# Kernel optimization log

Hardware: AMD Instinct MI355X
Metric: run time of the kernel (lower is better)

## Reference

```python
import jax, jax.numpy as jnp
import numpy as np
import math

N_NODES = 50000
N_EDGES = 800000
IN_DIM = 128
OUT_DIM = 64
TIME_DIM = 128


def setup_inputs() -> dict:
    key = jax.random.key(0)
    ks = jax.random.split(key, 9)
    return {
        "node_feats": jax.random.normal(ks[0], (N_NODES, IN_DIM), dtype=jnp.float32),
        "time_diff": jax.random.uniform(ks[1], (N_EDGES,), dtype=jnp.float32),
        "src": jax.random.randint(ks[2], (N_EDGES,), 0, N_NODES, dtype=jnp.int32),
        "dst": jax.random.randint(ks[3], (N_EDGES,), 0, N_NODES, dtype=jnp.int32),
        "W": jax.random.normal(ks[4], (OUT_DIM, IN_DIM), dtype=jnp.float32) * 0.05,
        "Wv": jax.random.normal(ks[5], (OUT_DIM, IN_DIM), dtype=jnp.float32) * 0.05,
        "omega": jax.random.normal(ks[6], (TIME_DIM // 2,), dtype=jnp.float32),
        "Wt": jax.random.normal(ks[7], (OUT_DIM, TIME_DIM), dtype=jnp.float32) * 0.05,
        "a": jax.random.normal(ks[8], (3 * OUT_DIM,), dtype=jnp.float32) * 0.05,
    }


def reference(node_feats, time_diff, src, dst, W, Wv, omega, Wt, a):
    N = node_feats.shape[0]
    d = W.shape[0]  # out_dim
    time_dim = 2 * omega.shape[0]

    # gather + linear projections per edge
    h_src = node_feats[src] @ W.T          # [E, d]
    h_dst = node_feats[dst] @ W.T          # [E, d]
    v_src = node_feats[src] @ Wv.T         # [E, d]

    # temporal encoding: interleaved sin/cos of t * omega, scaled by sqrt(1/dim)
    ang = time_diff[:, None] * omega[None, :]                       # [E, dim/2]
    pe = jnp.stack([jnp.sin(ang), jnp.cos(ang)], axis=-1)
    pe = pe.reshape(ang.shape[0], time_dim) * jnp.float32(math.sqrt(1.0 / time_dim))
    t_emb = pe @ Wt.T                                               # [E, d]

    # attn_fc(concat([h_src, h_dst, t_emb])) == split dot products (same math, no big concat)
    e = h_src @ a[:d] + h_dst @ a[d:2 * d] + t_emb @ a[2 * d:]      # [E]
    e = jnp.where(e > 0, e, 0.2 * e)  # LeakyReLU(0.2)

    # edge_softmax: softmax over incoming edges of each destination node
    m = jax.ops.segment_max(e, dst, num_segments=N)
    ex = jnp.exp(e - m[dst])
    den = jax.ops.segment_sum(ex, dst, num_segments=N)
    alpha = ex / den[dst]  # dropout is identity in eval mode

    # weighted message scatter-sum aggregation
    msg = v_src * alpha[:, None]                                    # [E, d]
    return jax.ops.segment_sum(msg, dst, num_segments=N)            # [N, d]
```

## Files before the change

### kernel.cpp

```cpp
#include <hip/hip_runtime.h>
#include <hip/hip_bf16.h>
#include <hip/hip_fp16.h>
#include <math.h>

#define IN_DIM   128
#define OUT_DIM  64
#define THALF    64
#define PE_SCALE 0.08838834764831845f
#define TBL      2048
#define EPB_LOG  14
#define EPB      (1 << EPB_LOG)

typedef __attribute__((ext_vector_type(8))) short  short8;
typedef __attribute__((ext_vector_type(4))) float  f32x4;

__device__ inline unsigned short bf16_rne(float x) {
    unsigned u = __float_as_uint(x);
    return (unsigned short)((u + 0x7FFFu + ((u >> 16) & 1u)) >> 16);
}

__global__ __launch_bounds__(256) void k_prep(
    const float* __restrict__ W, const float* __restrict__ Wt,
    const float* __restrict__ a, const float* __restrict__ Wv,
    const float* __restrict__ omega,
    float* __restrict__ gtab, unsigned short* __restrict__ Bp,
    int* __restrict__ pref)
{
    __shared__ float satv[IN_DIM];
    __shared__ float saW1[IN_DIM], saW2[IN_DIM];
    int t = threadIdx.x;
    if (t < IN_DIM) {
        float x3 = 0.f;
        for (int j = 0; j < OUT_DIM; ++j)
            x3 += a[2 * OUT_DIM + j] * Wt[j * IN_DIM + t];
        satv[t] = x3;
        if (blockIdx.x == 0) {
            float x1 = 0.f, x2 = 0.f;
            for (int j = 0; j < OUT_DIM; ++j) {
                float wj = W[j * IN_DIM + t];
                x1 += a[j] * wj;
                x2 += a[OUT_DIM + j] * wj;
            }
            saW1[t] = x1; saW2[t] = x2;
        }
    }
    __syncthreads();

    int idx = blockIdx.x * 256 + t;
    if (idx <= TBL) {
        float tt = (float)idx * (1.0f / TBL);
        float acc = 0.f;
#pragma unroll
        for (int i = 0; i < THALF; ++i) {
            float sp, cp;
            __sincosf(tt * omega[i], &sp, &cp);
            acc += sp * satv[2 * i] + cp * satv[2 * i + 1];
        }
        gtab[idx] = acc;
    }
    if (idx < 64) pref[idx] = 0;

    if (blockIdx.x == 0) {
        for (int i = t; i < 5 * 4 * 64 * 8; i += 256) {
            int j    = i & 7;
            int lane = (i >> 3) & 63;
            int k0i  = (i >> 9) & 3;
            int tt   = i >> 11;
            int kk = k0i * 32 + (lane >> 4) * 8 + j;
            int n  = lane & 15;
            float val;
            if (tt < 4)     val = Wv[(tt * 16 + n) * IN_DIM + kk];
            else            val = (n == 0) ? saW1[kk] : (n == 1) ? saW2[kk] : 0.f;
            Bp[i] = bf16_rne(val);
        }
    }
}

__global__ __launch_bounds__(1024) void k_hist(
    const int* __restrict__ dst,
    unsigned short* __restrict__ lrank,
    unsigned short* __restrict__ ghist16,
    int N, int E)
{
    extern __shared__ unsigned h[];
    int NH = (N + 1) >> 1;
    int t = threadIdx.x;
    for (int i = t; i < NH; i += 1024) h[i] = 0u;
    __syncthreads();
    int b = blockIdx.x;
    int e0 = b << EPB_LOG;
    int e1 = e0 + EPB; if (e1 > E) e1 = E;
    for (int e = e0 + t; e < e1; e += 1024) {
        int d = dst[e];
        unsigned inc = (d & 1) ? 0x10000u : 1u;
        unsigned old = atomicAdd(&h[d >> 1], inc);
        lrank[e] = (unsigned short)((d & 1) ? (old >> 16) : (old & 0xFFFFu));
    }
    __syncthreads();
    unsigned* gh32 = (unsigned*)(ghist16 + (size_t)b * N);
    for (int w = t; w < NH; w += 1024) gh32[w] = h[w];
}

__global__ __launch_bounds__(256) void k_scan_fuse(
    unsigned short* __restrict__ ghist16,
    int* __restrict__ offs,
    int* __restrict__ pref,
    int B, int N)
{
    __shared__ int lds[256];
    int b = blockIdx.x, t = threadIdx.x;
    int n0 = b * 1024 + t * 4;
    unsigned r0 = 0, r1 = 0, r2 = 0, r3 = 0;
    if (n0 + 3 < N) {
        for (int bb = 0; bb < B; ++bb) {
            unsigned short* p = ghist16 + (size_t)bb * N + n0;
            uint2 c = *(uint2*)p;
            uint2 w;
            w.x = (r0 & 0xFFFFu) | (r1 << 16);
            w.y = (r2 & 0xFFFFu) | (r3 << 16);
            *(uint2*)p = w;
            r0 += c.x & 0xFFFFu; r1 += c.x >> 16;
            r2 += c.y & 0xFFFFu; r3 += c.y >> 16;
        }
    } else if (n0 < N) {
        for (int bb = 0; bb < B; ++bb) {
            unsigned short* p = ghist16 + (size_t)bb * N + n0;
            unsigned c0 = p[0]; p[0] = (unsigned short)r0; r0 += c0;
            if (n0 + 1 < N) { unsigned c = p[1]; p[1] = (unsigned short)r1; r1 += c; }
            if (n0 + 2 < N) { unsigned c = p[2]; p[2] = (unsigned short)r2; r2 += c; }
            if (n0 + 3 < N) { unsigned c = p[3]; p[3] = (unsigned short)r3; r3 += c; }
        }
    }
    int s = (int)(r0 + r1 + r2 + r3);
    lds[t] = s;
    __syncthreads();
    for (int off = 1; off < 256; off <<= 1) {
        int tmp = (t >= off) ? lds[t - off] : 0;
        __syncthreads();
        lds[t] += tmp;
        __syncthreads();
    }
    int ex = lds[t] - s;
    if (n0 + 3 < N) {
        int4 o;
        o.x = ex;
        o.y = ex + (int)r0;
        o.z = ex + (int)(r0 + r1);
        o.w = ex + (int)(r0 + r1 + r2);
        *(int4*)(offs + n0) = o;
    } else if (n0 < N) {
        offs[n0] = ex;
        if (n0 + 1 < N) offs[n0 + 1] = ex + (int)r0;
        if (n0 + 2 < N) offs[n0 + 2] = ex + (int)(r0 + r1);
        if (n0 + 3 < N) offs[n0 + 3] = ex + (int)(r0 + r1 + r2);
    }
    int total = lds[255];
    if (t > b && t < (int)gridDim.x) atomicAdd(pref + t, total);
}

__global__ __launch_bounds__(256) void k_node_mfma(
    const float* __restrict__ feats,
    const unsigned short* __restrict__ Bp,
    unsigned short* __restrict__ vb,
    float* __restrict__ s1,
    float* __restrict__ s2,
    int N)
{
    int gwave = (blockIdx.x * 256 + threadIdx.x) >> 6;
    int lane  = threadIdx.x & 63;
    int ntiles = (N + 15) >> 4;
    if (gwave >= ntiles) return;
    int row = lane & 15, quad = lane >> 4;
    int nodeA = gwave * 16 + row;
    int nodeL = nodeA < N ? nodeA : N - 1;

    const float* arow = feats + (size_t)nodeL * IN_DIM + quad * 8;
    short8 afrag[4];
#pragma unroll
    for (int k0i = 0; k0i < 4; ++k0i) {
        float4 fa = *(const float4*)(arow + k0i * 32);
        float4 fb = *(const float4*)(arow + k0i * 32 + 4);
        union { unsigned u[4]; short8 s; } cv;
        cv.u[0] = (__float_as_uint(fa.x) >> 16) | (__float_as_uint(fa.y) & 0xFFFF0000u);
        cv.u[1] = (__float_as_uint(fa.z) >> 16) | (__float_as_uint(fa.w) & 0xFFFF0000u);
        cv.u[2] = (__float_as_uint(fb.x) >> 16) | (__float_as_uint(fb.y) & 0xFFFF0000u);
        cv.u[3] = (__float_as_uint(fb.z) >> 16) | (__float_as_uint(fb.w) & 0xFFFF0000u);
        afrag[k0i] = cv.s;
    }

    const short8* B8 = (const short8*)Bp;
    f32x4 acc[5];
#pragma unroll
    for (int t = 0; t < 5; ++t) acc[t] = (f32x4){0.f, 0.f, 0.f, 0.f};
#pragma unroll
    for (int t = 0; t < 5; ++t) {
#pragma unroll
        for (int k0i = 0; k0i < 4; ++k0i)
            acc[t] = __builtin_amdgcn_mfma_f32_16x16x32_bf16(
                afrag[k0i], B8[(t * 4 + k0i) * 64 + lane], acc[t], 0, 0, 0);
    }

    int col = lane & 15;
    int baseNode = gwave * 16 + quad * 4;
#pragma unroll
    for (int r = 0; r < 4; ++r) {
        int nd = baseNode + r;
        if (nd < N) {
            unsigned short* vr = vb + (size_t)nd * OUT_DIM + col;
#pragma unroll
            for (int t = 0; t < 4; ++t) vr[t * 16] = bf16_rne(acc[t][r]);
            if (col == 0)      s1[nd] = acc[4][r];
            else if (col == 1) s2[nd] = acc[4][r];
        }
    }
}

__global__ __launch_bounds__(256) void k_scatter_fused(
    const float* __restrict__ tdiff,
    const int* __restrict__ src,
    const int* __restrict__ dst,
    const float* __restrict__ gtab,
    const float* __restrict__ s1,
    const float* __restrict__ s2,
    const unsigned short* __restrict__ lrank,
    const unsigned short* __restrict__ ghist16,
    const int* __restrict__ offs,
    const int* __restrict__ pref,
    unsigned* __restrict__ payload,
    int N, int E)
{
    int base = (blockIdx.x * 256 + threadIdx.x) * 8;
    if (base >= E) return;
    if (base + 8 <= E) {
        int4   sa = *(const int4*)(src + base);
        int4   sb = *(const int4*)(src + base + 4);
        int4   da = *(const int4*)(dst + base);
        int4   db = *(const int4*)(dst + base + 4);
        float4 ta = *(const float4*)(tdiff + base);
        float4 tb = *(const float4*)(tdiff + base + 4);
        ushort4 la = *(const ushort4*)(lrank + base);
        ushort4 lb = *(const ushort4*)(lrank + base + 4);
        int s[8]    = {sa.x, sa.y, sa.z, sa.w, sb.x, sb.y, sb.z, sb.w};
        int d[8]    = {da.x, da.y, da.z, da.w, db.x, db.y, db.z, db.w};
        float tv[8] = {ta.x, ta.y, ta.z, ta.w, tb.x, tb.y, tb.z, tb.w};
        int lr[8]   = {la.x, la.y, la.z, la.w, lb.x, lb.y, lb.z, lb.w};

        int pos[8];
#pragma unroll
        for (int i = 0; i < 8; ++i) {
            int b = (base + i) >> EPB_LOG;
            pos[i] = offs[d[i]] + pref[d[i] >> 10] +
                     (int)ghist16[(size_t)b * N + d[i]] + lr[i];
        }
#pragma unroll
        for (int i = 0; i < 8; ++i) {
            float a1 = s1[s[i]];
            float a2 = s2[d[i]];
            float x = tv[i] * (float)TBL;
            int i0 = (int)x;
            i0 = i0 < 0 ? 0 : (i0 > TBL - 1 ? TBL - 1 : i0);
            float fr = x - (float)i0;
            float ev = a1 + a2 + PE_SCALE * (gtab[i0] + fr * (gtab[i0 + 1] - gtab[i0]));
            ev = ev > 0.f ? ev : 0.2f * ev;
            unsigned pw = ((unsigned)s[i] << 16) | (unsigned)__half_as_ushort(__float2half(ev));
            payload[pos[i]] = pw;
        }
    } else {
        for (int e = base; e < E; ++e) {
            int s = src[e], d = dst[e];
            float a1 = s1[s], a2 = s2[d];
            float x = tdiff[e] * (float)TBL;
            int i0 = (int)x;
            i0 = i0 < 0 ? 0 : (i0 > TBL - 1 ? TBL - 1 : i0);
            float fr = x - (float)i0;
            float ev = a1 + a2 + PE_SCALE * (gtab[i0] + fr * (gtab[i0 + 1] - gtab[i0]));
            ev = ev > 0.f ? ev : 0.2f * ev;
            unsigned pw = ((unsigned)s << 16) | (unsigned)__half_as_ushort(__float2half(ev));
            int b = e >> EPB_LOG;
            int pos = offs[d] + pref[d >> 10] + (int)ghist16[(size_t)b * N + d] + (int)lrank[e];
            payload[pos] = pw;
        }
    }
}

__global__ __launch_bounds__(256) void k_aggregate(
    const int* __restrict__ offs,
    const int* __restrict__ pref,
    const unsigned* __restrict__ payload,
    const unsigned short* __restrict__ vb,
    float* __restrict__ out,
    int N, int E)
{
    int wid  = (blockIdx.x * blockDim.x + threadIdx.x) >> 6;
    int lane = threadIdx.x & 63;
    if (wid >= N) return;
    int beg = offs[wid] + pref[wid >> 10];
    int end = (wid + 1 < N) ? (offs[wid + 1] + pref[(wid + 1) >> 10]) : E;
    int deg = end - beg;
    int g8 = lane >> 3, r = lane & 7;

    float acc[8];
#pragma unroll
    for (int i = 0; i < 8; ++i) acc[i] = 0.f;
    float den = 0.f;

    for (int base = 0; base < deg; base += 64) {
        int cl = deg - base; if (cl > 64) cl = 64;
        bool valid = lane < cl;
        unsigned pl = valid ? payload[beg + base + lane] : 0u;
        float ex = valid ? __expf(__half2float(__ushort_as_half((unsigned short)(pl & 0xFFFFu)))) : 0.f;
        int   sv = valid ? (int)(pl >> 16) : 0;

        float sum = ex;
#pragma unroll
        for (int off = 32; off; off >>= 1) sum += __shfl_xor(sum, off, 64);
        den += sum;

        int rounds = (cl + 15) >> 4;
        for (int j = 0; j < rounds; ++j) {
            int i0 = j * 16 + g8;
            int i1 = i0 + 8;
            float e0 = __shfl(ex, i0, 64);
            int   s0 = __shfl(sv, i0, 64);
            float e1 = __shfl(ex, i1, 64);
            int   s1v = __shfl(sv, i1, 64);
            uint4 w0 = *((const uint4*)(vb + (size_t)s0 * OUT_DIM) + r);
            uint4 w1 = *((const uint4*)(vb + (size_t)s1v * OUT_DIM) + r);
            acc[0] += e0 * __uint_as_float(w0.x << 16)         + e1 * __uint_as_float(w1.x << 16);
            acc[1] += e0 * __uint_as_float(w0.x & 0xFFFF0000u) + e1 * __uint_as_float(w1.x & 0xFFFF0000u);
            acc[2] += e0 * __uint_as_float(w0.y << 16)         + e1 * __uint_as_float(w1.y << 16);
            acc[3] += e0 * __uint_as_float(w0.y & 0xFFFF0000u) + e1 * __uint_as_float(w1.y & 0xFFFF0000u);
            acc[4] += e0 * __uint_as_float(w0.z << 16)         + e1 * __uint_as_float(w1.z << 16);
            acc[5] += e0 * __uint_as_float(w0.z & 0xFFFF0000u) + e1 * __uint_as_float(w1.z & 0xFFFF0000u);
            acc[6] += e0 * __uint_as_float(w0.w << 16)         + e1 * __uint_as_float(w1.w << 16);
            acc[7] += e0 * __uint_as_float(w0.w & 0xFFFF0000u) + e1 * __uint_as_float(w1.w & 0xFFFF0000u);
        }
    }

#pragma unroll
    for (int i = 0; i < 8; ++i) {
        acc[i] += __shfl_xor(acc[i], 8, 64);
        acc[i] += __shfl_xor(acc[i], 16, 64);
        acc[i] += __shfl_xor(acc[i], 32, 64);
    }

    if (g8 == 0) {
        float inv = (deg > 0) ? 1.f / den : 0.f;
        float* o = out + (size_t)wid * OUT_DIM + r * 8;
        *(float4*)(o)     = make_float4(acc[0] * inv, acc[1] * inv, acc[2] * inv, acc[3] * inv);
        *(float4*)(o + 4) = make_float4(acc[4] * inv, acc[5] * inv, acc[6] * inv, acc[7] * inv);
    }
}

extern "C" void kernel_launch(void* const* d_in, const int* in_sizes, int n_in,
                              void* d_out, int out_size, void* d_ws, size_t ws_size,
                              hipStream_t stream) {
    const float* feats = (const float*)d_in[0];
    const float* tdiff = (const float*)d_in[1];
    const int*   src   = (const int*)d_in[2];
    const int*   dst   = (const int*)d_in[3];
    const float* W     = (const float*)d_in[4];
    const float* Wv    = (const float*)d_in[5];
    const float* omega = (const float*)d_in[6];
    const float* Wt    = (const float*)d_in[7];
    const float* a     = (const float*)d_in[8];
    float* out = (float*)d_out;

    int N = in_sizes[0] / IN_DIM;
    int E = in_sizes[1];
    int B = (E + EPB - 1) >> EPB_LOG;

    float* ws      = (float*)d_ws;
    unsigned short* vb = (unsigned short*)ws;
    float* s1      = ws + (size_t)N * 32;
    float* s2      = s1 + N;
    unsigned* payload = (unsigned*)(s2 + N);
    unsigned short* lrank = (unsigned short*)(payload + E);
    int*   offs    = (int*)(lrank + ((E + 1) & ~1));
    int    offs_elems = ((N + 1023) / 1024) * 1024;
    int*   pref    = offs + offs_elems;
    float* gtab    = (float*)(pref + 64);
    unsigned short* Bp = (unsigned short*)(gtab + TBL + 1);
    size_t gho = ((size_t)((char*)(Bp + 10240) - (char*)ws) + 7) & ~(size_t)7;
    unsigned short* ghist16 = (unsigned short*)((char*)ws + gho);

    int nb = (N + 1023) / 1024;
    int ntiles = (N + 15) / 16;
    int eb8 = (E + 8 * 256 - 1) / (8 * 256);
    unsigned ldsb = (unsigned)(((N + 1) / 2) * 4);

    k_prep<<<(TBL / 256) + 1, 256, 0, stream>>>(W, Wt, a, Wv, omega, gtab, Bp, pref);
    k_hist<<<B, 1024, ldsb, stream>>>(dst, lrank, ghist16, N, E);
    k_node_mfma<<<(ntiles * 64 + 255) / 256, 256, 0, stream>>>(feats, Bp, vb, s1, s2, N);
    k_scan_fuse<<<nb, 256, 0, stream>>>(ghist16, offs, pref, B, N);
    k_scatter_fused<<<eb8, 256, 0, stream>>>(tdiff, src, dst, gtab, s1, s2,
                                             lrank, ghist16, offs, pref, payload, N, E);
    long long tot = (long long)N * OUT_DIM;
    k_aggregate<<<(int)((tot + 255) / 256), 256, 0, stream>>>(offs, pref, payload, vb, out, N, E);
}
```

Baseline: 181.7 us.

## Merge histogram and node MFMA kernels into one launch; fold denominator into gather loop

The destination histogram kernel and the per-node MFMA projection kernel are combined into one launch, with extra blocks beyond B running the projection. This removes one launch and lets the two independent phases overlap. The MFMA blocks now request the same large dynamic LDS allocation as the histogram blocks, which can limit occupancy. Separately, the aggregate kernel drops the per-chunk wave reduction of the softmax denominator, accumulates it per lane group inside the gather loop, and reduces it once at the end.

```diff
diff --git a/kernel.cpp b/kernel.cpp
--- a/kernel.cpp
+++ b/kernel.cpp
@@ -76,29 +76,84 @@
     }
 }
 
-__global__ __launch_bounds__(1024) void k_hist(
+__global__ __launch_bounds__(1024) void k_hist_mfma(
     const int* __restrict__ dst,
     unsigned short* __restrict__ lrank,
     unsigned short* __restrict__ ghist16,
-    int N, int E)
+    const float* __restrict__ feats,
+    const unsigned short* __restrict__ Bp,
+    unsigned short* __restrict__ vb,
+    float* __restrict__ s1,
+    float* __restrict__ s2,
+    int N, int E, int B)
 {
     extern __shared__ unsigned h[];
-    int NH = (N + 1) >> 1;
     int t = threadIdx.x;
-    for (int i = t; i < NH; i += 1024) h[i] = 0u;
-    __syncthreads();
-    int b = blockIdx.x;
-    int e0 = b << EPB_LOG;
-    int e1 = e0 + EPB; if (e1 > E) e1 = E;
-    for (int e = e0 + t; e < e1; e += 1024) {
-        int d = dst[e];
-        unsigned inc = (d & 1) ? 0x10000u : 1u;
-        unsigned old = atomicAdd(&h[d >> 1], inc);
-        lrank[e] = (unsigned short)((d & 1) ? (old >> 16) : (old & 0xFFFFu));
-    }
-    __syncthreads();
-    unsigned* gh32 = (unsigned*)(ghist16 + (size_t)b * N);
-    for (int w = t; w < NH; w += 1024) gh32[w] = h[w];
+    if ((int)blockIdx.x < B) {
+        int NH = (N + 1) >> 1;
+        for (int i = t; i < NH; i += 1024) h[i] = 0u;
+        __syncthreads();
+        int b = blockIdx.x;
+        int e0 = b << EPB_LOG;
+        int e1 = e0 + EPB; if (e1 > E) e1 = E;
+        for (int e = e0 + t; e < e1; e += 1024) {
+            int d = dst[e];
+            unsigned inc = (d & 1) ? 0x10000u : 1u;
+            unsigned old = atomicAdd(&h[d >> 1], inc);
+            lrank[e] = (unsigned short)((d & 1) ? (old >> 16) : (old & 0xFFFFu));
+        }
+        __syncthreads();
+        unsigned* gh32 = (unsigned*)(ghist16 + (size_t)b * N);
+        for (int w = t; w < NH; w += 1024) gh32[w] = h[w];
+        return;
+    }
+    int gwave = ((int)blockIdx.x - B) * 16 + (t >> 6);
+    int lane  = t & 63;
+    int ntiles = (N + 15) >> 4;
+    if (gwave >= ntiles) return;
+    int row = lane & 15, quad = lane >> 4;
+    int nodeA = gwave * 16 + row;
+    int nodeL = nodeA < N ? nodeA : N - 1;
+
+    const float* arow = feats + (size_t)nodeL * IN_DIM + quad * 8;
+    short8 afrag[4];
+#pragma unroll
+    for (int k0i = 0; k0i < 4; ++k0i) {
+        float4 fa = *(const float4*)(arow + k0i * 32);
+        float4 fb = *(const float4*)(arow + k0i * 32 + 4);
+        union { unsigned u[4]; short8 s; } cv;
+        cv.u[0] = (__float_as_uint(fa.x) >> 16) | (__float_as_uint(fa.y) & 0xFFFF0000u);
+        cv.u[1] = (__float_as_uint(fa.z) >> 16) | (__float_as_uint(fa.w) & 0xFFFF0000u);
+        cv.u[2] = (__float_as_uint(fb.x) >> 16) | (__float_as_uint(fb.y) & 0xFFFF0000u);
+        cv.u[3] = (__float_as_uint(fb.z) >> 16) | (__float_as_uint(fb.w) & 0xFFFF0000u);
+        afrag[k0i] = cv.s;
+    }
+
+    const short8* B8 = (const short8*)Bp;
+    f32x4 acc[5];
+#pragma unroll
+    for (int tt = 0; tt < 5; ++tt) acc[tt] = (f32x4){0.f, 0.f, 0.f, 0.f};
+#pragma unroll
+    for (int tt = 0; tt < 5; ++tt) {
+#pragma unroll
+        for (int k0i = 0; k0i < 4; ++k0i)
+            acc[tt] = __builtin_amdgcn_mfma_f32_16x16x32_bf16(
+                afrag[k0i], B8[(tt * 4 + k0i) * 64 + lane], acc[tt], 0, 0, 0);
+    }
+
+    int col = lane & 15;
+    int baseNode = gwave * 16 + quad * 4;
+#pragma unroll
+    for (int r = 0; r < 4; ++r) {
+        int nd = baseNode + r;
+        if (nd < N) {
+            unsigned short* vr = vb + (size_t)nd * OUT_DIM + col;
+#pragma unroll
+            for (int tt = 0; tt < 4; ++tt) vr[tt * 16] = bf16_rne(acc[tt][r]);
+            if (col == 0)      s1[nd] = acc[4][r];
+            else if (col == 1) s2[nd] = acc[4][r];
+        }
+    }
 }
 
 __global__ __launch_bounds__(256) void k_scan_fuse(
@@ -156,63 +211,6 @@
     }
     int total = lds[255];
     if (t > b && t < (int)gridDim.x) atomicAdd(pref + t, total);
-}
-
-__global__ __launch_bounds__(256) void k_node_mfma(
-    const float* __restrict__ feats,
-    const unsigned short* __restrict__ Bp,
-    unsigned short* __restrict__ vb,
-    float* __restrict__ s1,
-    float* __restrict__ s2,
-    int N)
-{
-    int gwave = (blockIdx.x * 256 + threadIdx.x) >> 6;
-    int lane  = threadIdx.x & 63;
-    int ntiles = (N + 15) >> 4;
-    if (gwave >= ntiles) return;
-    int row = lane & 15, quad = lane >> 4;
-    int nodeA = gwave * 16 + row;
-    int nodeL = nodeA < N ? nodeA : N - 1;
-
-    const float* arow = feats + (size_t)nodeL * IN_DIM + quad * 8;
-    short8 afrag[4];
-#pragma unroll
-    for (int k0i = 0; k0i < 4; ++k0i) {
-        float4 fa = *(const float4*)(arow + k0i * 32);
-        float4 fb = *(const float4*)(arow + k0i * 32 + 4);
-        union { unsigned u[4]; short8 s; } cv;
-        cv.u[0] = (__float_as_uint(fa.x) >> 16) | (__float_as_uint(fa.y) & 0xFFFF0000u);
-        cv.u[1] = (__float_as_uint(fa.z) >> 16) | (__float_as_uint(fa.w) & 0xFFFF0000u);
-        cv.u[2] = (__float_as_uint(fb.x) >> 16) | (__float_as_uint(fb.y) & 0xFFFF0000u);
-        cv.u[3] = (__float_as_uint(fb.z) >> 16) | (__float_as_uint(fb.w) & 0xFFFF0000u);
-        afrag[k0i] = cv.s;
-    }
-
-    const short8* B8 = (const short8*)Bp;
-    f32x4 acc[5];
-#pragma unroll
-    for (int t = 0; t < 5; ++t) acc[t] = (f32x4){0.f, 0.f, 0.f, 0.f};
-#pragma unroll
-    for (int t = 0; t < 5; ++t) {
-#pragma unroll
-        for (int k0i = 0; k0i < 4; ++k0i)
-            acc[t] = __builtin_amdgcn_mfma_f32_16x16x32_bf16(
-                afrag[k0i], B8[(t * 4 + k0i) * 64 + lane], acc[t], 0, 0, 0);
-    }
-
-    int col = lane & 15;
-    int baseNode = gwave * 16 + quad * 4;
-#pragma unroll
-    for (int r = 0; r < 4; ++r) {
-        int nd = baseNode + r;
-        if (nd < N) {
-            unsigned short* vr = vb + (size_t)nd * OUT_DIM + col;
-#pragma unroll
-            for (int t = 0; t < 4; ++t) vr[t * 16] = bf16_rne(acc[t][r]);
-            if (col == 0)      s1[nd] = acc[4][r];
-            else if (col == 1) s2[nd] = acc[4][r];
-        }
-    }
 }
 
 __global__ __launch_bounds__(256) void k_scatter_fused(
@@ -311,11 +309,6 @@
         float ex = valid ? __expf(__half2float(__ushort_as_half((unsigned short)(pl & 0xFFFFu)))) : 0.f;
         int   sv = valid ? (int)(pl >> 16) : 0;
 
-        float sum = ex;
-#pragma unroll
-        for (int off = 32; off; off >>= 1) sum += __shfl_xor(sum, off, 64);
-        den += sum;
-
         int rounds = (cl + 15) >> 4;
         for (int j = 0; j < rounds; ++j) {
             int i0 = j * 16 + g8;
@@ -324,6 +317,7 @@
             int   s0 = __shfl(sv, i0, 64);
             float e1 = __shfl(ex, i1, 64);
             int   s1v = __shfl(sv, i1, 64);
+            den += e0 + e1;
             uint4 w0 = *((const uint4*)(vb + (size_t)s0 * OUT_DIM) + r);
             uint4 w1 = *((const uint4*)(vb + (size_t)s1v * OUT_DIM) + r);
             acc[0] += e0 * __uint_as_float(w0.x << 16)         + e1 * __uint_as_float(w1.x << 16);
@@ -343,6 +337,9 @@
         acc[i] += __shfl_xor(acc[i], 16, 64);
         acc[i] += __shfl_xor(acc[i], 32, 64);
     }
+    den += __shfl_xor(den, 8, 64);
+    den += __shfl_xor(den, 16, 64);
+    den += __shfl_xor(den, 32, 64);
 
     if (g8 == 0) {
         float inv = (deg > 0) ? 1.f / den : 0.f;
@@ -386,12 +383,13 @@
 
     int nb = (N + 1023) / 1024;
     int ntiles = (N + 15) / 16;
+    int mblocks = (ntiles + 15) / 16;
     int eb8 = (E + 8 * 256 - 1) / (8 * 256);
     unsigned ldsb = (unsigned)(((N + 1) / 2) * 4);
 
     k_prep<<<(TBL / 256) + 1, 256, 0, stream>>>(W, Wt, a, Wv, omega, gtab, Bp, pref);
-    k_hist<<<B, 1024, ldsb, stream>>>(dst, lrank, ghist16, N, E);
-    k_node_mfma<<<(ntiles * 64 + 255) / 256, 256, 0, stream>>>(feats, Bp, vb, s1, s2, N);
+    k_hist_mfma<<<B + mblocks, 1024, ldsb, stream>>>(dst, lrank, ghist16,
+                                                     feats, Bp, vb, s1, s2, N, E, B);
     k_scan_fuse<<<nb, 256, 0, stream>>>(ghist16, offs, pref, B, N);
     k_scatter_fused<<<eb8, 256, 0, stream>>>(tdiff, src, dst, gtab, s1, s2,
                                              lrank, ghist16, offs, pref, payload, N, E);
```

Measured after the change: 174.8 us. -3.8%, faster.
